# Optimization experiments

Hardware: AMD Instinct MI355X
Metric: run time of the kernel (lower is better)

Reference implementation:

```python
import jax, jax.numpy as jnp
import numpy as np

N_NODES = 50000
N_EDGES = 600000
IN_DIM = 128
HID = 128
N_CLASSES = 40
N_GRAPHS = 128


def setup_inputs() -> dict:
    key = jax.random.key(0)
    ks = jax.random.split(key, 12)
    x = jax.random.normal(ks[0], (N_NODES, IN_DIM), dtype=jnp.float32)
    edge_index = jax.random.randint(ks[1], (2, N_EDGES), 0, N_NODES, dtype=jnp.int64)
    batch = jnp.sort(jax.random.randint(ks[2], (N_NODES,), 0, N_GRAPHS, dtype=jnp.int64))
    dims = [IN_DIM, HID, HID, N_CLASSES]
    params = {}
    for l in range(3):
        d_in, d_out = dims[l], dims[l + 1]
        s = 1.0 / np.sqrt(d_in)
        params[f"Wl{l}"] = jax.random.uniform(ks[3 + 3 * l], (d_out, d_in), jnp.float32, -s, s)
        params[f"bl{l}"] = jax.random.uniform(ks[4 + 3 * l], (d_out,), jnp.float32, -s, s)
        params[f"Wr{l}"] = jax.random.uniform(ks[5 + 3 * l], (d_out, d_in), jnp.float32, -s, s)
    return {"x": x, "edge_index": edge_index, "batch": batch, **params}


def _sage_layer(h, src, dst, Wl, bl, Wr):
    # message: relu(x_j) (edge_attr is None -> zero), mean-aggregate at dst
    m = jnp.maximum(h[src], 0.0)                       # [E, d]
    agg = jax.ops.segment_sum(m, dst, num_segments=N_NODES)
    cnt = jax.ops.segment_sum(jnp.ones((m.shape[0],), h.dtype), dst, num_segments=N_NODES)
    agg = agg / jnp.maximum(cnt, 1.0)[:, None]
    # lin_l(agg) + lin_r(x)
    return agg @ Wl.T + bl + h @ Wr.T


def reference(x, edge_index, batch, Wl0, bl0, Wr0, Wl1, bl1, Wr1, Wl2, bl2, Wr2):
    src, dst = edge_index[0], edge_index[1]
    Ws = [(Wl0, bl0, Wr0), (Wl1, bl1, Wr1), (Wl2, bl2, Wr2)]
    h = x
    for l, (Wl, bl, Wr) in enumerate(Ws):
        # dropout is identity in eval mode
        h = _sage_layer(h, src, dst, Wl, bl, Wr)
        if l != len(Ws) - 1:
            h = jnp.maximum(h, 0.0)
    # global mean pool over graphs
    gsum = jax.ops.segment_sum(h, batch, num_segments=N_GRAPHS)
    gcnt = jax.ops.segment_sum(jnp.ones((h.shape[0],), h.dtype), batch, num_segments=N_GRAPHS)
    g = gsum / jnp.maximum(gcnt, 1.0)[:, None]
    return h, g
```

## Files before the change

kernel.cpp:

```cpp
#include <hip/hip_runtime.h>
#include <hip/hip_bf16.h>


#define NODES 50000
#define K_DIM 128
#define N_GRAPHS 128

typedef __attribute__((ext_vector_type(8))) short short8;
typedef __attribute__((ext_vector_type(4))) short short4v;
typedef __attribute__((ext_vector_type(4))) float f32x4;

__device__ inline short f2bf(float f) {
    unsigned u = __builtin_bit_cast(unsigned, f);
    u += 0x7FFFu + ((u >> 16) & 1u);
    return (short)(u >> 16);
}
__device__ inline float bf2f(short h) {
    unsigned u = ((unsigned)(unsigned short)h) << 16;
    return __builtin_bit_cast(float, u);
}
__device__ inline unsigned hilo_pack(float f) {
    short h = f2bf(f);
    short l = f2bf(f - bf2f(h));
    return ((unsigned)(unsigned short)h) | (((unsigned)(unsigned short)l) << 16);
}

__global__ void init_kernel(const float* __restrict__ w0, const float* __restrict__ w1,
                            const float* __restrict__ w2, const float* __restrict__ w3,
                            const float* __restrict__ w4, const float* __restrict__ w5,
                            short* __restrict__ whi, short* __restrict__ wlo,
                            int* __restrict__ deg, const int* __restrict__ batch,
                            int* __restrict__ gstart, int N) {
    int idx = blockIdx.x * 256 + threadIdx.x;
    if (idx < N) deg[idx] = 0;
    const int TOT = 4 * 16384 + 96 * 128;
    if (idx < TOT) {
        float v;
        if (idx < 65536) {
            int m = idx >> 14, e = idx & 16383;
            const float* W = (m == 0) ? w0 : (m == 1) ? w1 : (m == 2) ? w2 : w3;
            v = W[e];
        } else {
            int i2 = idx - 65536;
            int row = i2 >> 7, col = i2 & 127;
            if (row < 40)      v = w4[row * 128 + col];
            else if (row < 80) v = w5[(row - 40) * 128 + col];
            else               v = 0.f;
        }
        unsigned p = hilo_pack(v);
        whi[idx] = (short)(p & 0xFFFFu);
        wlo[idx] = (short)(p >> 16);
    }
    if (idx <= N_GRAPHS) {
        int g = idx;
        int lo = 0, hi = N;
        while (lo < hi) {
            int mid = (lo + hi) >> 1;
            if (batch[mid] < g) lo = mid + 1; else hi = mid;
        }
        gstart[g] = lo;
    }
}

__global__ void deg_kernel(const int* __restrict__ dst, int* __restrict__ deg, int E) {
    int e = blockIdx.x * blockDim.x + threadIdx.x;
    if (e < E) atomicAdd(&deg[dst[e]], 1);
}

__global__ void scan_p1(const int* __restrict__ deg, int* __restrict__ bsum, int N) {
    int i = blockIdx.x * 256 + threadIdx.x;
    int v = (i < N) ? deg[i] : 0;
    #pragma unroll
    for (int off = 32; off > 0; off >>= 1) v += __shfl_down(v, off, 64);
    __shared__ int ws[4];
    int lane = threadIdx.x & 63, wv = threadIdx.x >> 6;
    if (lane == 0) ws[wv] = v;
    __syncthreads();
    if (threadIdx.x == 0) bsum[blockIdx.x] = ws[0] + ws[1] + ws[2] + ws[3];
}

__global__ void scan_p2(int* __restrict__ bsum, int NB) {
    int tid = threadIdx.x, lane = tid & 63, wv = tid >> 6;
    int v = (tid < NB) ? bsum[tid] : 0;
    int incl = v;
    #pragma unroll
    for (int off = 1; off < 64; off <<= 1) {
        int t = __shfl_up(incl, off, 64);
        if (lane >= off) incl += t;
    }
    __shared__ int ws[4];
    if (lane == 63) ws[wv] = incl;
    __syncthreads();
    int add = 0;
    for (int i = 0; i < wv; ++i) add += ws[i];
    incl += add;
    if (tid < NB) bsum[tid] = incl - v;
}

__global__ void scan_p3(const int* __restrict__ deg, const int* __restrict__ boff,
                        int* __restrict__ rowptr, int* __restrict__ fillpos, int N) {
    int i = blockIdx.x * 256 + threadIdx.x;
    int tid = threadIdx.x, lane = tid & 63, wv = tid >> 6;
    int v = (i < N) ? deg[i] : 0;
    int incl = v;
    #pragma unroll
    for (int off = 1; off < 64; off <<= 1) {
        int t = __shfl_up(incl, off, 64);
        if (lane >= off) incl += t;
    }
    __shared__ int ws[4];
    if (lane == 63) ws[wv] = incl;
    __syncthreads();
    int add = 0;
    for (int k = 0; k < wv; ++k) add += ws[k];
    int excl = boff[blockIdx.x] + incl + add - v;
    if (i < N) { rowptr[i] = excl; fillpos[i] = excl; }
    if (i == N) rowptr[N] = excl;
}

__global__ void fill_kernel(const int* __restrict__ src, const int* __restrict__ dst,
                            int* __restrict__ fillpos, int* __restrict__ csr_src, int E) {
    int e = blockIdx.x * blockDim.x + threadIdx.x;
    if (e < E) {
        int p = atomicAdd(&fillpos[dst[e]], 1);
        csr_src[p] = src[e];
    }
}

template <bool RELU>
__global__ void agg_kernel(const float* __restrict__ h, const int* __restrict__ rowptr,
                           const int* __restrict__ csr_src, float* __restrict__ agg, int N) {
    int w = (blockIdx.x * blockDim.x + threadIdx.x) >> 6;
    if (w >= N) return;
    int lane = threadIdx.x & 63;
    int half = lane >> 5, l32 = lane & 31;
    int s = rowptr[w], e = rowptr[w + 1];
    float4 acc = make_float4(0.f, 0.f, 0.f, 0.f);
    int i = s + half;
    for (; i + 6 < e; i += 8) {
        int s0 = csr_src[i], s1 = csr_src[i + 2], s2 = csr_src[i + 4], s3 = csr_src[i + 6];
        float4 v0 = reinterpret_cast<const float4*>(h + (size_t)s0 * K_DIM)[l32];
        float4 v1 = reinterpret_cast<const float4*>(h + (size_t)s1 * K_DIM)[l32];
        float4 v2 = reinterpret_cast<const float4*>(h + (size_t)s2 * K_DIM)[l32];
        float4 v3 = reinterpret_cast<const float4*>(h + (size_t)s3 * K_DIM)[l32];
        if (RELU) {
            acc.x += fmaxf(v0.x, 0.f) + fmaxf(v1.x, 0.f) + fmaxf(v2.x, 0.f) + fmaxf(v3.x, 0.f);
            acc.y += fmaxf(v0.y, 0.f) + fmaxf(v1.y, 0.f) + fmaxf(v2.y, 0.f) + fmaxf(v3.y, 0.f);
            acc.z += fmaxf(v0.z, 0.f) + fmaxf(v1.z, 0.f) + fmaxf(v2.z, 0.f) + fmaxf(v3.z, 0.f);
            acc.w += fmaxf(v0.w, 0.f) + fmaxf(v1.w, 0.f) + fmaxf(v2.w, 0.f) + fmaxf(v3.w, 0.f);
        } else {
            acc.x += v0.x + v1.x + v2.x + v3.x;
            acc.y += v0.y + v1.y + v2.y + v3.y;
            acc.z += v0.z + v1.z + v2.z + v3.z;
            acc.w += v0.w + v1.w + v2.w + v3.w;
        }
    }
    for (; i < e; i += 2) {
        int s0 = csr_src[i];
        float4 v0 = reinterpret_cast<const float4*>(h + (size_t)s0 * K_DIM)[l32];
        if (RELU) {
            acc.x += fmaxf(v0.x, 0.f); acc.y += fmaxf(v0.y, 0.f);
            acc.z += fmaxf(v0.z, 0.f); acc.w += fmaxf(v0.w, 0.f);
        } else {
            acc.x += v0.x; acc.y += v0.y; acc.z += v0.z; acc.w += v0.w;
        }
    }
    acc.x += __shfl_xor(acc.x, 32, 64);
    acc.y += __shfl_xor(acc.y, 32, 64);
    acc.z += __shfl_xor(acc.z, 32, 64);
    acc.w += __shfl_xor(acc.w, 32, 64);
    if (half == 0) {
        float inv = 1.0f / fmaxf((float)(e - s), 1.0f);
        acc.x *= inv; acc.y *= inv; acc.z *= inv; acc.w *= inv;
        reinterpret_cast<float4*>(agg + (size_t)w * K_DIM)[l32] = acc;
    }
}

template <int WAVES_M, int WAVES_N, int WM_TILES, int WN_TILES, int DOUT, bool RELU,
          int PHASES, bool BIAS>
__global__ __launch_bounds__(256) void sage_mfma(
        const float* __restrict__ A, const float* __restrict__ H,
        const short* __restrict__ Bhl, const short* __restrict__ Bll,
        const short* __restrict__ Bhr, const short* __restrict__ Blr,
        const float* __restrict__ bl, float* __restrict__ out, int N) {
    constexpr int BM = WAVES_M * WM_TILES * 16;
    constexpr int LSTR = 40;
    const int tid = threadIdx.x;
    const int lane = tid & 63;
    const int wave = tid >> 6;
    const int wm = wave % WAVES_M;
    const int wn = wave / WAVES_M;
    const int l15 = lane & 15;
    const int quad = lane >> 4;
    const int m0 = blockIdx.x * BM;

    __shared__ __align__(16) short Ahi[BM * LSTR];
    __shared__ __align__(16) short Alo[BM * LSTR];

    f32x4 acc[WM_TILES][WN_TILES];
    #pragma unroll
    for (int i = 0; i < WM_TILES; ++i)
        #pragma unroll
        for (int j = 0; j < WN_TILES; ++j)
            acc[i][j] = (f32x4){0.f, 0.f, 0.f, 0.f};

    #pragma unroll
    for (int ph = 0; ph < PHASES; ++ph) {
        const float* __restrict__ X = ph ? H : A;
        const short* __restrict__ Bh = ph ? Bhr : Bhl;
        const short* __restrict__ Bv = ph ? Blr : Bll;
        for (int k0 = 0; k0 < K_DIM; k0 += 32) {
            __syncthreads();
            #pragma unroll
            for (int r = 0; r < BM * 8 / 256; ++r) {
                int idx = r * 256 + tid;
                int row = idx >> 3, c4 = idx & 7;
                int m = m0 + row;
                float4 v = make_float4(0.f, 0.f, 0.f, 0.f);
                if (m < N) v = *reinterpret_cast<const float4*>(X + (size_t)m * K_DIM + k0 + c4 * 4);
                unsigned px = hilo_pack(v.x);
                unsigned py = hilo_pack(v.y);
                unsigned pz = hilo_pack(v.z);
                unsigned pw = hilo_pack(v.w);
                short4v h4, l4;
                h4[0] = (short)(px & 0xFFFFu); l4[0] = (short)(px >> 16);
                h4[1] = (short)(py & 0xFFFFu); l4[1] = (short)(py >> 16);
                h4[2] = (short)(pz & 0xFFFFu); l4[2] = (short)(pz >> 16);
                h4[3] = (short)(pw & 0xFFFFu); l4[3] = (short)(pw >> 16);
                *reinterpret_cast<short4v*>(&Ahi[row * LSTR + c4 * 4]) = h4;
                *reinterpret_cast<short4v*>(&Alo[row * LSTR + c4 * 4]) = l4;
            }
            short8 bh[WN_TILES], bo[WN_TILES];
            #pragma unroll
            for (int nt = 0; nt < WN_TILES; ++nt) {
                int n = wn * WN_TILES * 16 + nt * 16 + l15;
                bh[nt] = *reinterpret_cast<const short8*>(Bh + (size_t)n * K_DIM + k0 + quad * 8);
                bo[nt] = *reinterpret_cast<const short8*>(Bv + (size_t)n * K_DIM + k0 + quad * 8);
            }
            __syncthreads();
            #pragma unroll
            for (int mt = 0; mt < WM_TILES; ++mt) {
                int row = wm * WM_TILES * 16 + mt * 16 + l15;
                short8 ah = *reinterpret_cast<const short8*>(&Ahi[row * LSTR + quad * 8]);
                short8 ao = *reinterpret_cast<const short8*>(&Alo[row * LSTR + quad * 8]);
                #pragma unroll
                for (int nt = 0; nt < WN_TILES; ++nt) {
                    acc[mt][nt] = __builtin_amdgcn_mfma_f32_16x16x32_bf16(ah, bh[nt], acc[mt][nt], 0, 0, 0);
                    acc[mt][nt] = __builtin_amdgcn_mfma_f32_16x16x32_bf16(ah, bo[nt], acc[mt][nt], 0, 0, 0);
                    acc[mt][nt] = __builtin_amdgcn_mfma_f32_16x16x32_bf16(ao, bh[nt], acc[mt][nt], 0, 0, 0);
                }
            }
        }
    }

    float bias[WN_TILES];
    #pragma unroll
    for (int nt = 0; nt < WN_TILES; ++nt) {
        int col = wn * WN_TILES * 16 + nt * 16 + l15;
        bias[nt] = (BIAS && col < DOUT) ? bl[col] : 0.f;
    }
    #pragma unroll
    for (int mt = 0; mt < WM_TILES; ++mt) {
        #pragma unroll
        for (int nt = 0; nt < WN_TILES; ++nt) {
            int col = wn * WN_TILES * 16 + nt * 16 + l15;
            #pragma unroll
            for (int reg = 0; reg < 4; ++reg) {
                int row = m0 + wm * WM_TILES * 16 + mt * 16 + quad * 4 + reg;
                if (row < N && col < DOUT) {
                    float v = acc[mt][nt][reg] + bias[nt];
                    if (RELU) v = fmaxf(v, 0.f);
                    out[(size_t)row * DOUT + col] = v;
                }
            }
        }
    }
}

__global__ __launch_bounds__(256) void gemm80(
        const float* __restrict__ X, const short* __restrict__ Bh,
        const short* __restrict__ Bv, const float* __restrict__ b2,
        float* __restrict__ out, int N) {
    constexpr int BM = 64;
    constexpr int LSTR = 40;
    const int tid = threadIdx.x;
    const int lane = tid & 63;
    const int wave = tid >> 6;
    const int wm = wave & 1;
    const int wn = wave >> 1;
    const int l15 = lane & 15;
    const int quad = lane >> 4;
    const int m0 = blockIdx.x * BM;

    __shared__ __align__(16) short Ahi[BM * LSTR];
    __shared__ __align__(16) short Alo[BM * LSTR];

    f32x4 acc[2][3];
    #pragma unroll
    for (int i = 0; i < 2; ++i)
        #pragma unroll
        for (int j = 0; j < 3; ++j) acc[i][j] = (f32x4){0.f, 0.f, 0.f, 0.f};

    for (int k0 = 0; k0 < K_DIM; k0 += 32) {
        __syncthreads();
        #pragma unroll
        for (int r = 0; r < 2; ++r) {
            int idx = r * 256 + tid;
            int row = idx >> 3, c4 = idx & 7;
            int m = m0 + row;
            float4 v = make_float4(0.f, 0.f, 0.f, 0.f);
            if (m < N) v = *reinterpret_cast<const float4*>(X + (size_t)m * K_DIM + k0 + c4 * 4);
            unsigned px = hilo_pack(v.x);
            unsigned py = hilo_pack(v.y);
            unsigned pz = hilo_pack(v.z);
            unsigned pw = hilo_pack(v.w);
            short4v h4, l4;
            h4[0] = (short)(px & 0xFFFFu); l4[0] = (short)(px >> 16);
            h4[1] = (short)(py & 0xFFFFu); l4[1] = (short)(py >> 16);
            h4[2] = (short)(pz & 0xFFFFu); l4[2] = (short)(pz >> 16);
            h4[3] = (short)(pw & 0xFFFFu); l4[3] = (short)(pw >> 16);
            *reinterpret_cast<short4v*>(&Ahi[row * LSTR + c4 * 4]) = h4;
            *reinterpret_cast<short4v*>(&Alo[row * LSTR + c4 * 4]) = l4;
        }
        __syncthreads();
        short8 bh[3], bo[3];
        #pragma unroll
        for (int nt = 0; nt < 3; ++nt) {
            int n = wn * 48 + nt * 16 + l15;
            bh[nt] = *reinterpret_cast<const short8*>(Bh + (size_t)n * K_DIM + k0 + quad * 8);
            bo[nt] = *reinterpret_cast<const short8*>(Bv + (size_t)n * K_DIM + k0 + quad * 8);
        }
        #pragma unroll
        for (int mt = 0; mt < 2; ++mt) {
            int row = wm * 32 + mt * 16 + l15;
            short8 ah = *reinterpret_cast<const short8*>(&Ahi[row * LSTR + quad * 8]);
            short8 ao = *reinterpret_cast<const short8*>(&Alo[row * LSTR + quad * 8]);
            #pragma unroll
            for (int nt = 0; nt < 3; ++nt) {
                acc[mt][nt] = __builtin_amdgcn_mfma_f32_16x16x32_bf16(ah, bh[nt], acc[mt][nt], 0, 0, 0);
                acc[mt][nt] = __builtin_amdgcn_mfma_f32_16x16x32_bf16(ah, bo[nt], acc[mt][nt], 0, 0, 0);
                acc[mt][nt] = __builtin_amdgcn_mfma_f32_16x16x32_bf16(ao, bh[nt], acc[mt][nt], 0, 0, 0);
            }
        }
    }

    #pragma unroll
    for (int mt = 0; mt < 2; ++mt) {
        #pragma unroll
        for (int nt = 0; nt < 3; ++nt) {
            int col = wn * 48 + nt * 16 + l15;
            float b = (col >= 40 && col < 80) ? b2[col - 40] : 0.f;
            #pragma unroll
            for (int reg = 0; reg < 4; ++reg) {
                int row = m0 + wm * 32 + mt * 16 + quad * 4 + reg;
                if (row < N && col < 80) {
                    out[(size_t)row * 80 + col] = acc[mt][nt][reg] + b;
                }
            }
        }
    }
}

__global__ void agg40_kernel(const float* __restrict__ y80,
                             const int* __restrict__ rowptr, const int* __restrict__ csr_src,
                             float* __restrict__ out, int N) {
    int w = (blockIdx.x * blockDim.x + threadIdx.x) >> 6;
    if (w >= N) return;
    int lane = threadIdx.x & 63;
    int s = rowptr[w], e = rowptr[w + 1];
    if (lane >= 40) return;
    float acc = 0.f;
    int i = s;
    for (; i + 3 < e; i += 4) {
        int s0 = csr_src[i], s1 = csr_src[i + 1], s2 = csr_src[i + 2], s3 = csr_src[i + 3];
        float v0 = y80[(size_t)s0 * 80 + lane];
        float v1 = y80[(size_t)s1 * 80 + lane];
        float v2 = y80[(size_t)s2 * 80 + lane];
        float v3 = y80[(size_t)s3 * 80 + lane];
        acc += (v0 + v1) + (v2 + v3);
    }
    for (; i < e; ++i) acc += y80[(size_t)csr_src[i] * 80 + lane];
    float inv = 1.0f / fmaxf((float)(e - s), 1.0f);
    out[(size_t)w * 40 + lane] = acc * inv + y80[(size_t)w * 80 + 40 + lane];
}

__global__ __launch_bounds__(320) void pool_kernel(const float* __restrict__ h,
                                                   const int* __restrict__ gstart,
                                                   float* __restrict__ g_out) {
    int g = blockIdx.x;
    int tid = threadIdx.x;
    int c = tid % 40, r = tid / 40;
    int s = gstart[g], e = gstart[g + 1];
    float acc = 0.f;
    for (int n = s + r; n < e; n += 8)
        acc += h[(size_t)n * 40 + c];
    __shared__ float sh[8][40];
    sh[r][c] = acc;
    __syncthreads();
    if (r == 0) {
        float sum = 0.f;
        #pragma unroll
        for (int i = 0; i < 8; ++i) sum += sh[i][c];
        g_out[g * 40 + c] = sum / fmaxf((float)(e - s), 1.0f);
    }
}

extern "C" void kernel_launch(void* const* d_in, const int* in_sizes, int n_in,
                              void* d_out, int out_size, void* d_ws, size_t ws_size,
                              hipStream_t stream) {
    const float* x    = (const float*)d_in[0];
    const int*   ei   = (const int*)d_in[1];
    const int*   batch= (const int*)d_in[2];
    const float* Wl0  = (const float*)d_in[3];
    const float* bl0  = (const float*)d_in[4];
    const float* Wr0  = (const float*)d_in[5];
    const float* Wl1  = (const float*)d_in[6];
    const float* bl1  = (const float*)d_in[7];
    const float* Wr1  = (const float*)d_in[8];
    const float* Wl2  = (const float*)d_in[9];
    const float* bl2  = (const float*)d_in[10];
    const float* Wr2  = (const float*)d_in[11];

    const int N = in_sizes[0] / K_DIM;
    const int E = in_sizes[1] / 2;
    const int* src = ei;
    const int* dst = ei + E;

    float* out = (float*)d_out;
    float* gsum = out + (size_t)N * 40;

    char* w = (char*)d_ws;
    auto alloc = [&](size_t bytes) {
        char* p = w;
        w += (bytes + 255) & ~(size_t)255;
        return p;
    };
    float* bufA  = (float*)alloc((size_t)N * K_DIM * 4);
    float* bufB  = (float*)alloc((size_t)N * K_DIM * 4);
    float* bufC  = (float*)alloc((size_t)N * K_DIM * 4);
    float* y80   = (float*)alloc((size_t)N * 80 * 4);
    int*   rowptr= (int*)alloc((size_t)(N + 1) * 4);
    int*   deg   = (int*)alloc((size_t)N * 4);
    int*   fillp = (int*)alloc((size_t)N * 4);
    int*   csr   = (int*)alloc((size_t)E * 4);
    int*   bsum  = (int*)alloc(256 * 4);
    int*   gstart= (int*)alloc((size_t)(N_GRAPHS + 1) * 4);
    short* whi   = (short*)alloc(77824 * 2);
    short* wlo   = (short*)alloc(77824 * 2);

    const int NB = (N + 255) / 256;
    const int initGrid = (77824 + 255) / 256;

    init_kernel<<<initGrid, 256, 0, stream>>>(Wl0, Wr0, Wl1, Wr1, Wl2, Wr2,
                                              whi, wlo, deg, batch, gstart, N);
    deg_kernel<<<(E + 255) / 256, 256, 0, stream>>>(dst, deg, E);
    scan_p1<<<NB, 256, 0, stream>>>(deg, bsum, N);
    scan_p2<<<1, 256, 0, stream>>>(bsum, NB);
    scan_p3<<<NB, 256, 0, stream>>>(deg, bsum, rowptr, fillp, N);
    fill_kernel<<<(E + 255) / 256, 256, 0, stream>>>(src, dst, fillp, csr, E);

    short* hWl0 = whi;          short* lWl0 = wlo;
    short* hWr0 = whi + 16384;  short* lWr0 = wlo + 16384;
    short* hWl1 = whi + 32768;  short* lWl1 = wlo + 32768;
    short* hWr1 = whi + 49152;  short* lWr1 = wlo + 49152;
    short* hW2  = whi + 65536;  short* lW2  = wlo + 65536;

    const int aggGrid  = (N * 64 + 255) / 256;
    const int gemmGrid = (N + 63) / 64;

    agg_kernel<true><<<aggGrid, 256, 0, stream>>>(x, rowptr, csr, bufA, N);
    sage_mfma<1, 4, 4, 2, 128, true, 2, true><<<gemmGrid, 256, 0, stream>>>(
        bufA, x, hWl0, lWl0, hWr0, lWr0, bl0, bufB, N);
    agg_kernel<false><<<aggGrid, 256, 0, stream>>>(bufB, rowptr, csr, bufA, N);
    sage_mfma<1, 4, 4, 2, 128, true, 2, true><<<gemmGrid, 256, 0, stream>>>(
        bufA, bufB, hWl1, lWl1, hWr1, lWr1, bl1, bufC, N);
    gemm80<<<gemmGrid, 256, 0, stream>>>(bufC, hW2, lW2, bl2, y80, N);
    agg40_kernel<<<aggGrid, 256, 0, stream>>>(y80, rowptr, csr, out, N);

    pool_kernel<<<N_GRAPHS, 320, 0, stream>>>(out, gstart, gsum);
}
```

Before: 359.6 us.

## Gather neighbor features in bf16 for all aggregation passes and merge scan kernels

Stores bf16 copies of the ReLU'd input, the layer-1 output and the left half of the final projection, and has the three aggregation kernels gather these instead of fp32 rows. This halves the bytes moved by the bandwidth-bound random gathers. It also fuses the two scan passes into one kernel and splits the y80 buffer into a bf16 part and an fp32 part. The cost is an extra conversion pass over x in init, extra bf16 stores in the GEMM epilogue, and bf16 rounding of the aggregated messages, which reduces accuracy.

```diff
diff --git a/kernel.cpp b/kernel.cpp
--- a/kernel.cpp
+++ b/kernel.cpp
@@ -19,6 +19,8 @@
     unsigned u = ((unsigned)(unsigned short)h) << 16;
     return __builtin_bit_cast(float, u);
 }
+__device__ inline float blo(unsigned u) { return __builtin_bit_cast(float, u << 16); }
+__device__ inline float bhi(unsigned u) { return __builtin_bit_cast(float, u & 0xFFFF0000u); }
 __device__ inline unsigned hilo_pack(float f) {
     short h = f2bf(f);
     short l = f2bf(f - bf2f(h));
@@ -30,8 +32,18 @@
                             const float* __restrict__ w4, const float* __restrict__ w5,
                             short* __restrict__ whi, short* __restrict__ wlo,
                             int* __restrict__ deg, const int* __restrict__ batch,
-                            int* __restrict__ gstart, int N) {
+                            int* __restrict__ gstart,
+                            const float* __restrict__ x, short* __restrict__ xb, int N) {
     int idx = blockIdx.x * 256 + threadIdx.x;
+    if (idx < N * (K_DIM / 4)) {
+        float4 v = reinterpret_cast<const float4*>(x)[idx];
+        short4v b;
+        b[0] = f2bf(fmaxf(v.x, 0.f));
+        b[1] = f2bf(fmaxf(v.y, 0.f));
+        b[2] = f2bf(fmaxf(v.z, 0.f));
+        b[3] = f2bf(fmaxf(v.w, 0.f));
+        *reinterpret_cast<short4v*>(&xb[idx * 4]) = b;
+    }
     if (idx < N) deg[idx] = 0;
     const int TOT = 4 * 16384 + 96 * 128;
     if (idx < TOT) {
@@ -79,41 +91,42 @@
     if (threadIdx.x == 0) bsum[blockIdx.x] = ws[0] + ws[1] + ws[2] + ws[3];
 }
 
-__global__ void scan_p2(int* __restrict__ bsum, int NB) {
-    int tid = threadIdx.x, lane = tid & 63, wv = tid >> 6;
-    int v = (tid < NB) ? bsum[tid] : 0;
+__global__ void scan_p23(const int* __restrict__ deg, const int* __restrict__ bsum,
+                         int* __restrict__ rowptr, int* __restrict__ fillpos,
+                         int N, int NB) {
+    const int tid = threadIdx.x, lane = tid & 63, wv = tid >> 6;
+    __shared__ int ws[4];
+    __shared__ int sboff[256];
+    {
+        int v = (tid < NB) ? bsum[tid] : 0;
+        int incl = v;
+        #pragma unroll
+        for (int off = 1; off < 64; off <<= 1) {
+            int t = __shfl_up(incl, off, 64);
+            if (lane >= off) incl += t;
+        }
+        if (lane == 63) ws[wv] = incl;
+        __syncthreads();
+        int add = 0;
+        for (int k = 0; k < wv; ++k) add += ws[k];
+        sboff[tid] = incl + add - v;
+        __syncthreads();
+    }
+    const int boff = sboff[blockIdx.x];
+    int i = blockIdx.x * 256 + tid;
+    int v = (i < N) ? deg[i] : 0;
     int incl = v;
     #pragma unroll
     for (int off = 1; off < 64; off <<= 1) {
         int t = __shfl_up(incl, off, 64);
         if (lane >= off) incl += t;
     }
-    __shared__ int ws[4];
-    if (lane == 63) ws[wv] = incl;
+    __shared__ int ws2[4];
+    if (lane == 63) ws2[wv] = incl;
     __syncthreads();
     int add = 0;
-    for (int i = 0; i < wv; ++i) add += ws[i];
-    incl += add;
-    if (tid < NB) bsum[tid] = incl - v;
-}
-
-__global__ void scan_p3(const int* __restrict__ deg, const int* __restrict__ boff,
-                        int* __restrict__ rowptr, int* __restrict__ fillpos, int N) {
-    int i = blockIdx.x * 256 + threadIdx.x;
-    int tid = threadIdx.x, lane = tid & 63, wv = tid >> 6;
-    int v = (i < N) ? deg[i] : 0;
-    int incl = v;
-    #pragma unroll
-    for (int off = 1; off < 64; off <<= 1) {
-        int t = __shfl_up(incl, off, 64);
-        if (lane >= off) incl += t;
-    }
-    __shared__ int ws[4];
-    if (lane == 63) ws[wv] = incl;
-    __syncthreads();
-    int add = 0;
-    for (int k = 0; k < wv; ++k) add += ws[k];
-    int excl = boff[blockIdx.x] + incl + add - v;
+    for (int k = 0; k < wv; ++k) add += ws2[k];
+    int excl = boff + incl + add - v;
     if (i < N) { rowptr[i] = excl; fillpos[i] = excl; }
     if (i == N) rowptr[N] = excl;
 }
@@ -127,9 +140,10 @@
     }
 }
 
-template <bool RELU>
-__global__ void agg_kernel(const float* __restrict__ h, const int* __restrict__ rowptr,
-                           const int* __restrict__ csr_src, float* __restrict__ agg, int N) {
+__global__ void agg_bf16(const unsigned short* __restrict__ hb,
+                         const int* __restrict__ rowptr,
+                         const int* __restrict__ csr_src,
+                         float* __restrict__ agg, int N) {
     int w = (blockIdx.x * blockDim.x + threadIdx.x) >> 6;
     if (w >= N) return;
     int lane = threadIdx.x & 63;
@@ -139,31 +153,20 @@
     int i = s + half;
     for (; i + 6 < e; i += 8) {
         int s0 = csr_src[i], s1 = csr_src[i + 2], s2 = csr_src[i + 4], s3 = csr_src[i + 6];
-        float4 v0 = reinterpret_cast<const float4*>(h + (size_t)s0 * K_DIM)[l32];
-        float4 v1 = reinterpret_cast<const float4*>(h + (size_t)s1 * K_DIM)[l32];
-        float4 v2 = reinterpret_cast<const float4*>(h + (size_t)s2 * K_DIM)[l32];
-        float4 v3 = reinterpret_cast<const float4*>(h + (size_t)s3 * K_DIM)[l32];
-        if (RELU) {
-            acc.x += fmaxf(v0.x, 0.f) + fmaxf(v1.x, 0.f) + fmaxf(v2.x, 0.f) + fmaxf(v3.x, 0.f);
-            acc.y += fmaxf(v0.y, 0.f) + fmaxf(v1.y, 0.f) + fmaxf(v2.y, 0.f) + fmaxf(v3.y, 0.f);
-            acc.z += fmaxf(v0.z, 0.f) + fmaxf(v1.z, 0.f) + fmaxf(v2.z, 0.f) + fmaxf(v3.z, 0.f);
-            acc.w += fmaxf(v0.w, 0.f) + fmaxf(v1.w, 0.f) + fmaxf(v2.w, 0.f) + fmaxf(v3.w, 0.f);
-        } else {
-            acc.x += v0.x + v1.x + v2.x + v3.x;
-            acc.y += v0.y + v1.y + v2.y + v3.y;
-            acc.z += v0.z + v1.z + v2.z + v3.z;
-            acc.w += v0.w + v1.w + v2.w + v3.w;
-        }
+        uint2 v0 = reinterpret_cast<const uint2*>(hb + (size_t)s0 * K_DIM)[l32];
+        uint2 v1 = reinterpret_cast<const uint2*>(hb + (size_t)s1 * K_DIM)[l32];
+        uint2 v2 = reinterpret_cast<const uint2*>(hb + (size_t)s2 * K_DIM)[l32];
+        uint2 v3 = reinterpret_cast<const uint2*>(hb + (size_t)s3 * K_DIM)[l32];
+        acc.x += (blo(v0.x) + blo(v1.x)) + (blo(v2.x) + blo(v3.x));
+        acc.y += (bhi(v0.x) + bhi(v1.x)) + (bhi(v2.x) + bhi(v3.x));
+        acc.z += (blo(v0.y) + blo(v1.y)) + (blo(v2.y) + blo(v3.y));
+        acc.w += (bhi(v0.y) + bhi(v1.y)) + (bhi(v2.y) + bhi(v3.y));
     }
     for (; i < e; i += 2) {
         int s0 = csr_src[i];
-        float4 v0 = reinterpret_cast<const float4*>(h + (size_t)s0 * K_DIM)[l32];
-        if (RELU) {
-            acc.x += fmaxf(v0.x, 0.f); acc.y += fmaxf(v0.y, 0.f);
-            acc.z += fmaxf(v0.z, 0.f); acc.w += fmaxf(v0.w, 0.f);
-        } else {
-            acc.x += v0.x; acc.y += v0.y; acc.z += v0.z; acc.w += v0.w;
-        }
+        uint2 v0 = reinterpret_cast<const uint2*>(hb + (size_t)s0 * K_DIM)[l32];
+        acc.x += blo(v0.x); acc.y += bhi(v0.x);
+        acc.z += blo(v0.y); acc.w += bhi(v0.y);
     }
     acc.x += __shfl_xor(acc.x, 32, 64);
     acc.y += __shfl_xor(acc.y, 32, 64);
@@ -176,13 +179,13 @@
     }
 }
 
-template <int WAVES_M, int WAVES_N, int WM_TILES, int WN_TILES, int DOUT, bool RELU,
-          int PHASES, bool BIAS>
+template <int WAVES_M, int WAVES_N, int WM_TILES, int WN_TILES, bool BF16OUT>
 __global__ __launch_bounds__(256) void sage_mfma(
         const float* __restrict__ A, const float* __restrict__ H,
         const short* __restrict__ Bhl, const short* __restrict__ Bll,
         const short* __restrict__ Bhr, const short* __restrict__ Blr,
-        const float* __restrict__ bl, float* __restrict__ out, int N) {
+        const float* __restrict__ bl, float* __restrict__ out,
+        short* __restrict__ outb, int N) {
     constexpr int BM = WAVES_M * WM_TILES * 16;
     constexpr int LSTR = 40;
     const int tid = threadIdx.x;
@@ -205,7 +208,7 @@
             acc[i][j] = (f32x4){0.f, 0.f, 0.f, 0.f};
 
     #pragma unroll
-    for (int ph = 0; ph < PHASES; ++ph) {
+    for (int ph = 0; ph < 2; ++ph) {
         const float* __restrict__ X = ph ? H : A;
         const short* __restrict__ Bh = ph ? Bhr : Bhl;
         const short* __restrict__ Bv = ph ? Blr : Bll;
@@ -253,24 +256,19 @@
         }
     }
 
-    float bias[WN_TILES];
-    #pragma unroll
-    for (int nt = 0; nt < WN_TILES; ++nt) {
-        int col = wn * WN_TILES * 16 + nt * 16 + l15;
-        bias[nt] = (BIAS && col < DOUT) ? bl[col] : 0.f;
-    }
     #pragma unroll
     for (int mt = 0; mt < WM_TILES; ++mt) {
         #pragma unroll
         for (int nt = 0; nt < WN_TILES; ++nt) {
             int col = wn * WN_TILES * 16 + nt * 16 + l15;
+            float b = bl[col];
             #pragma unroll
             for (int reg = 0; reg < 4; ++reg) {
                 int row = m0 + wm * WM_TILES * 16 + mt * 16 + quad * 4 + reg;
-                if (row < N && col < DOUT) {
-                    float v = acc[mt][nt][reg] + bias[nt];
-                    if (RELU) v = fmaxf(v, 0.f);
-                    out[(size_t)row * DOUT + col] = v;
+                if (row < N) {
+                    float v = fmaxf(acc[mt][nt][reg] + b, 0.f);
+                    out[(size_t)row * K_DIM + col] = v;
+                    if (BF16OUT) outb[(size_t)row * K_DIM + col] = f2bf(v);
                 }
             }
         }
@@ -280,7 +278,7 @@
 __global__ __launch_bounds__(256) void gemm80(
         const float* __restrict__ X, const short* __restrict__ Bh,
         const short* __restrict__ Bv, const float* __restrict__ b2,
-        float* __restrict__ out, int N) {
+        short* __restrict__ ylb, float* __restrict__ yr40, int N) {
     constexpr int BM = 64;
     constexpr int LSTR = 40;
     const int tid = threadIdx.x;
@@ -349,19 +347,24 @@
         #pragma unroll
         for (int nt = 0; nt < 3; ++nt) {
             int col = wn * 48 + nt * 16 + l15;
-            float b = (col >= 40 && col < 80) ? b2[col - 40] : 0.f;
             #pragma unroll
             for (int reg = 0; reg < 4; ++reg) {
                 int row = m0 + wm * 32 + mt * 16 + quad * 4 + reg;
-                if (row < N && col < 80) {
-                    out[(size_t)row * 80 + col] = acc[mt][nt][reg] + b;
+                if (row < N) {
+                    float v = acc[mt][nt][reg];
+                    if (col < 40) {
+                        ylb[(size_t)row * 40 + col] = f2bf(v);
+                    } else if (col < 80) {
+                        yr40[(size_t)row * 40 + (col - 40)] = v + b2[col - 40];
+                    }
                 }
             }
         }
     }
 }
 
-__global__ void agg40_kernel(const float* __restrict__ y80,
+__global__ void agg40_kernel(const unsigned short* __restrict__ ylb,
+                             const float* __restrict__ yr40,
                              const int* __restrict__ rowptr, const int* __restrict__ csr_src,
                              float* __restrict__ out, int N) {
     int w = (blockIdx.x * blockDim.x + threadIdx.x) >> 6;
@@ -373,15 +376,15 @@
     int i = s;
     for (; i + 3 < e; i += 4) {
         int s0 = csr_src[i], s1 = csr_src[i + 1], s2 = csr_src[i + 2], s3 = csr_src[i + 3];
-        float v0 = y80[(size_t)s0 * 80 + lane];
-        float v1 = y80[(size_t)s1 * 80 + lane];
-        float v2 = y80[(size_t)s2 * 80 + lane];
-        float v3 = y80[(size_t)s3 * 80 + lane];
+        float v0 = bf2f((short)ylb[(size_t)s0 * 40 + lane]);
+        float v1 = bf2f((short)ylb[(size_t)s1 * 40 + lane]);
+        float v2 = bf2f((short)ylb[(size_t)s2 * 40 + lane]);
+        float v3 = bf2f((short)ylb[(size_t)s3 * 40 + lane]);
         acc += (v0 + v1) + (v2 + v3);
     }
-    for (; i < e; ++i) acc += y80[(size_t)csr_src[i] * 80 + lane];
+    for (; i < e; ++i) acc += bf2f((short)ylb[(size_t)csr_src[i] * 40 + lane]);
     float inv = 1.0f / fmaxf((float)(e - s), 1.0f);
-    out[(size_t)w * 40 + lane] = acc * inv + y80[(size_t)w * 80 + 40 + lane];
+    out[(size_t)w * 40 + lane] = acc * inv + yr40[(size_t)w * 40 + lane];
 }
 
 __global__ __launch_bounds__(320) void pool_kernel(const float* __restrict__ h,
@@ -438,7 +441,8 @@
     float* bufA  = (float*)alloc((size_t)N * K_DIM * 4);
     float* bufB  = (float*)alloc((size_t)N * K_DIM * 4);
     float* bufC  = (float*)alloc((size_t)N * K_DIM * 4);
-    float* y80   = (float*)alloc((size_t)N * 80 * 4);
+    short* ylb   = (short*)alloc((size_t)N * 40 * 2);
+    float* yr40  = (float*)alloc((size_t)N * 40 * 4);
     int*   rowptr= (int*)alloc((size_t)(N + 1) * 4);
     int*   deg   = (int*)alloc((size_t)N * 4);
     int*   fillp = (int*)alloc((size_t)N * 4);
@@ -448,15 +452,17 @@
     short* whi   = (short*)alloc(77824 * 2);
     short* wlo   = (short*)alloc(77824 * 2);
 
+    short* xb  = (short*)bufC;
+    short* h1b = (short*)bufC + (size_t)N * K_DIM;
+
     const int NB = (N + 255) / 256;
-    const int initGrid = (77824 + 255) / 256;
+    const int initGrid = (N * (K_DIM / 4) + 255) / 256;
 
     init_kernel<<<initGrid, 256, 0, stream>>>(Wl0, Wr0, Wl1, Wr1, Wl2, Wr2,
-                                              whi, wlo, deg, batch, gstart, N);
+                                              whi, wlo, deg, batch, gstart, x, xb, N);
     deg_kernel<<<(E + 255) / 256, 256, 0, stream>>>(dst, deg, E);
     scan_p1<<<NB, 256, 0, stream>>>(deg, bsum, N);
-    scan_p2<<<1, 256, 0, stream>>>(bsum, NB);
-    scan_p3<<<NB, 256, 0, stream>>>(deg, bsum, rowptr, fillp, N);
+    scan_p23<<<NB, 256, 0, stream>>>(deg, bsum, rowptr, fillp, N, NB);
     fill_kernel<<<(E + 255) / 256, 256, 0, stream>>>(src, dst, fillp, csr, E);
 
     short* hWl0 = whi;          short* lWl0 = wlo;
@@ -468,14 +474,14 @@
     const int aggGrid  = (N * 64 + 255) / 256;
     const int gemmGrid = (N + 63) / 64;
 
-    agg_kernel<true><<<aggGrid, 256, 0, stream>>>(x, rowptr, csr, bufA, N);
-    sage_mfma<1, 4, 4, 2, 128, true, 2, true><<<gemmGrid, 256, 0, stream>>>(
-        bufA, x, hWl0, lWl0, hWr0, lWr0, bl0, bufB, N);
-    agg_kernel<false><<<aggGrid, 256, 0, stream>>>(bufB, rowptr, csr, bufA, N);
-    sage_mfma<1, 4, 4, 2, 128, true, 2, true><<<gemmGrid, 256, 0, stream>>>(
-        bufA, bufB, hWl1, lWl1, hWr1, lWr1, bl1, bufC, N);
-    gemm80<<<gemmGrid, 256, 0, stream>>>(bufC, hW2, lW2, bl2, y80, N);
-    agg40_kernel<<<aggGrid, 256, 0, stream>>>(y80, rowptr, csr, out, N);
+    agg_bf16<<<aggGrid, 256, 0, stream>>>((const unsigned short*)xb, rowptr, csr, bufA, N);
+    sage_mfma<1, 4, 4, 2, true><<<gemmGrid, 256, 0, stream>>>(
+        bufA, x, hWl0, lWl0, hWr0, lWr0, bl0, bufB, h1b, N);
+    agg_bf16<<<aggGrid, 256, 0, stream>>>((const unsigned short*)h1b, rowptr, csr, bufA, N);
+    sage_mfma<1, 4, 4, 2, false><<<gemmGrid, 256, 0, stream>>>(
+        bufA, bufB, hWl1, lWl1, hWr1, lWr1, bl1, bufC, nullptr, N);
+    gemm80<<<gemmGrid, 256, 0, stream>>>(bufC, hW2, lW2, bl2, ylb, yr40, N);
+    agg40_kernel<<<aggGrid, 256, 0, stream>>>((const unsigned short*)ylb, yr40, rowptr, csr, out, N);
 
     pool_kernel<<<N_GRAPHS, 320, 0, stream>>>(out, gstart, gsum);
 }
```

Result: faster. 337.0 us (-6.3%).
